# Kernel optimization log

Measured on AMD Instinct MI355X. Metric: run time of the kernel, lower is better.

## Reference

```python
import jax, jax.numpy as jnp
import numpy as np

N_NODES = 100000
N_EDGES = 1600000
N_GRAPHS = 64
NEG_SLOPE = 0.2


def gat_conv(x, W, att_src, att_dst, bias, edge_index, n_nodes, heads, out_ch, concat):
    """PyG-style GATConv (eval mode, self loops already included in edge_index)."""
    h = (x @ W).reshape(n_nodes, heads, out_ch)            # [N, H, C]
    a_src = jnp.einsum('nhc,hc->nh', h, att_src)           # [N, H]
    a_dst = jnp.einsum('nhc,hc->nh', h, att_dst)           # [N, H]
    src, dst = edge_index[0], edge_index[1]
    e = jax.nn.leaky_relu(a_src[src] + a_dst[dst], NEG_SLOPE)   # [E, H]
    # segment softmax over incoming edges of each destination node
    m = jax.ops.segment_max(e, dst, num_segments=n_nodes)      # [N, H]
    ex = jnp.exp(e - m[dst])
    denom = jax.ops.segment_sum(ex, dst, num_segments=n_nodes) # [N, H]
    alpha = ex / denom[dst]                                     # [E, H]
    msg = h[src] * alpha[:, :, None]                            # [E, H, C]
    out = jax.ops.segment_sum(msg, dst, num_segments=n_nodes)   # [N, H, C]
    if concat:
        out = out.reshape(n_nodes, heads * out_ch)
    else:
        out = out.mean(axis=1)
    return out + bias


def setup_inputs() -> dict:
    key = jax.random.key(0)
    ks = jax.random.split(key, 16)
    x = jax.random.normal(ks[0], (N_NODES, 1), dtype=jnp.float32)
    edge_index = jax.random.randint(ks[1], (2, N_EDGES), 0, N_NODES, dtype=jnp.int64)
    batch = jnp.sort(jax.random.randint(ks[2], (N_NODES,), 0, N_GRAPHS, dtype=jnp.int64))
    def glorot(k, shape):
        fan = (shape[0] + shape[-1])
        return jax.random.uniform(k, shape, jnp.float32, -1.0, 1.0) * np.sqrt(6.0 / fan)
    # layer 1: in=1, heads=8, out=8, concat
    W1 = glorot(ks[3], (1, 64))
    att_src1 = glorot(ks[4], (8, 8))
    att_dst1 = glorot(ks[5], (8, 8))
    b1 = jnp.zeros((64,), jnp.float32)
    # layer 2: in=64, heads=8, out=16, mean
    W2 = glorot(ks[6], (64, 128))
    att_src2 = glorot(ks[7], (8, 16))
    att_dst2 = glorot(ks[8], (8, 16))
    b2 = jnp.zeros((16,), jnp.float32)
    # fc 16 -> 4
    Wfc = glorot(ks[9], (16, 4))
    bfc = jnp.zeros((4,), jnp.float32)
    return dict(x=x, W1=W1, att_src1=att_src1, att_dst1=att_dst1, b1=b1,
                W2=W2, att_src2=att_src2, att_dst2=att_dst2, b2=b2,
                Wfc=Wfc, bfc=bfc, edge_index=edge_index, batch=batch)


def reference(x, W1, att_src1, att_dst1, b1, W2, att_src2, att_dst2, b2, Wfc, bfc, edge_index, batch):
    n = x.shape[0]
    # PyG GATConv default add_self_loops=True
    loops = jnp.arange(n, dtype=edge_index.dtype)
    ei = jnp.concatenate([edge_index, jnp.stack([loops, loops])], axis=1)
    h = gat_conv(x, W1, att_src1, att_dst1, b1, ei, n, heads=8, out_ch=8, concat=True)
    h = jax.nn.elu(h)
    # F.dropout(training=False) and attention dropout are no-ops in eval mode
    h = gat_conv(h, W2, att_src2, att_dst2, b2, ei, n, heads=8, out_ch=16, concat=False)
    # global mean pool over graphs
    sums = jax.ops.segment_sum(h, batch, num_segments=N_GRAPHS)          # [G, 16]
    cnts = jax.ops.segment_sum(jnp.ones((n,), h.dtype), batch, num_segments=N_GRAPHS)
    pooled = sums / jnp.maximum(cnts, 1.0)[:, None]
    return pooled @ Wfc + bfc                                            # [G, 4]
```

## Files before the change

kernel.cpp:

```cpp
#include <hip/hip_runtime.h>
#include <hip/hip_fp16.h>

#define N_NODES  100000
#define N_EDGES  1600000
#define N_GRAPHS 64

#define BINSH  8
#define NBIN   392
#define BINCAP 8192
#define EPB    2048
#define BUCKSH 13

__device__ __forceinline__ float lrelu(float v) { return v > 0.f ? v : 0.2f * v; }
__device__ __forceinline__ float elu_f(float v) { return v > 0.f ? v : __expf(v) - 1.f; }
__device__ __forceinline__ float rdlane_f(float v, int lane) {
    return __int_as_float(__builtin_amdgcn_readlane(__float_as_int(v), lane));
}

__global__ __launch_bounds__(512) void k_binA(
    const int* __restrict__ src, const int* __restrict__ dst,
    const int* __restrict__ batch, int* __restrict__ gbin_cursor,
    int* __restrict__ cnt, int2* __restrict__ binned) {
    __shared__ int hist[NBIN], lexcl[NBIN], runbase[NBIN], lcur[NBIN];
    __shared__ int wpart[8];
    __shared__ int gh[N_GRAPHS];
    __shared__ int2 stage[EPB];
    int t = threadIdx.x;
    int e0 = blockIdx.x * EPB;
    for (int b = t; b < NBIN; b += 512) hist[b] = 0;
    if (t < N_GRAPHS) gh[t] = 0;
    __syncthreads();
    int nid = blockIdx.x * 512 + t;
    if (nid < N_NODES) atomicAdd(&gh[batch[nid]], 1);
    int e = 4 * t;
    int4 dv = make_int4(0, 0, 0, 0), sv = make_int4(0, 0, 0, 0);
    bool full = (e0 + e + 3 < N_EDGES);
    if (full) {
        dv = *(const int4*)(dst + e0 + e);
        sv = *(const int4*)(src + e0 + e);
        atomicAdd(&hist[dv.x >> BINSH], 1);
        atomicAdd(&hist[dv.y >> BINSH], 1);
        atomicAdd(&hist[dv.z >> BINSH], 1);
        atomicAdd(&hist[dv.w >> BINSH], 1);
    } else {
        for (int k = 0; k < 4; ++k)
            if (e0 + e + k < N_EDGES) atomicAdd(&hist[dst[e0 + e + k] >> BINSH], 1);
    }
    __syncthreads();
    int v = (t < NBIN) ? hist[t] : 0;
    int x = v;
#pragma unroll
    for (int d = 1; d < 64; d <<= 1) {
        int y = __shfl_up(x, d, 64);
        if ((t & 63) >= d) x += y;
    }
    if ((t & 63) == 63) wpart[t >> 6] = x;
    __syncthreads();
    if (t == 0) {
        int a = 0;
        for (int w = 0; w < 8; ++w) { int q = wpart[w]; wpart[w] = a; a += q; }
    }
    __syncthreads();
    int excl = x - v + wpart[t >> 6];
    if (t < NBIN) { lexcl[t] = excl; lcur[t] = excl; }
    __syncthreads();
    if (t < NBIN && v > 0) runbase[t] = atomicAdd(&gbin_cursor[t], v);
    if (t < N_GRAPHS && gh[t]) atomicAdd(&cnt[t], gh[t]);
    __syncthreads();
    if (full) {
        int p;
        p = atomicAdd(&lcur[dv.x >> BINSH], 1); stage[p] = make_int2(sv.x, dv.x);
        p = atomicAdd(&lcur[dv.y >> BINSH], 1); stage[p] = make_int2(sv.y, dv.y);
        p = atomicAdd(&lcur[dv.z >> BINSH], 1); stage[p] = make_int2(sv.z, dv.z);
        p = atomicAdd(&lcur[dv.w >> BINSH], 1); stage[p] = make_int2(sv.w, dv.w);
    } else {
        for (int k = 0; k < 4; ++k) {
            if (e0 + e + k < N_EDGES) {
                int d = dst[e0 + e + k];
                int p = atomicAdd(&lcur[d >> BINSH], 1);
                stage[p] = make_int2(src[e0 + e + k], d);
            }
        }
    }
    __syncthreads();
    int m = N_EDGES - e0;
    if (m > EPB) m = EPB;
    for (int i = 4 * t; i < 4 * t + 4 && i < m; ++i) {
        int2 pr = stage[i];
        int b = pr.y >> BINSH;
        binned[(size_t)b * BINCAP + runbase[b] + (i - lexcl[b])] = pr;
    }
}

__global__ __launch_bounds__(1024) void k_binB(
    const int2* __restrict__ binned, const int* __restrict__ gbin_cursor,
    int* __restrict__ off, int* __restrict__ csr) {
    __shared__ int hist[4096];
    __shared__ int wpart[16];
    __shared__ int s_ebase;
    int b = blockIdx.x, t = threadIdx.x;
    int count = gbin_cursor[b];
    int node0 = b << BINSH;
    const int2* my = binned + (size_t)b * BINCAP;
    if (t == 0) s_ebase = 0;
    for (int i = t; i < 4096; i += 1024) hist[i] = 0;
    __syncthreads();
    if (t < b) atomicAdd(&s_ebase, gbin_cursor[t]);
    for (int i = t; i < count; i += 1024) {
        int2 pr = my[i];
        int key = ((pr.y - node0) << 4) | (pr.x >> BUCKSH);
        atomicAdd(&hist[key], 1);
    }
    __syncthreads();
    int v0 = hist[4 * t], v1 = hist[4 * t + 1], v2 = hist[4 * t + 2], v3 = hist[4 * t + 3];
    int s = v0 + v1 + v2 + v3;
    int x = s;
#pragma unroll
    for (int d = 1; d < 64; d <<= 1) {
        int y = __shfl_up(x, d, 64);
        if ((t & 63) >= d) x += y;
    }
    if ((t & 63) == 63) wpart[t >> 6] = x;
    __syncthreads();
    if (t == 0) {
        int a = 0;
        for (int w = 0; w < 16; ++w) { int q = wpart[w]; wpart[w] = a; a += q; }
    }
    __syncthreads();
    int base = x - s + wpart[t >> 6];
    hist[4 * t]     = base;
    hist[4 * t + 1] = base + v0;
    hist[4 * t + 2] = base + v0 + v1;
    hist[4 * t + 3] = base + v0 + v1 + v2;
    __syncthreads();
    int ebase = s_ebase;
    if (t < 256) {
        int n = node0 + t;
        if (n < N_NODES) off[n] = ebase + hist[t << 4];
    }
    if (b == 0 && t == 0) off[N_NODES] = N_EDGES;
    __syncthreads();
    for (int i = t; i < count; i += 1024) {
        int2 pr = my[i];
        int key = ((pr.y - node0) << 4) | (pr.x >> BUCKSH);
        int p = atomicAdd(&hist[key], 1);
        csr[ebase + p] = pr.x;
    }
}

__global__ __launch_bounds__(256) void k_l1gemm(
    const float* __restrict__ x, const float* __restrict__ W1,
    const float* __restrict__ as1, const float* __restrict__ ad1,
    const float* __restrict__ b1, const float* __restrict__ W2,
    const float* __restrict__ as2, const float* __restrict__ ad2,
    const int* __restrict__ off, const int* __restrict__ csr,
    __half2* __restrict__ h2p, float2* __restrict__ ap, float2* __restrict__ dp) {
    __shared__ float4 smW4[32 * 64];
    __shared__ float smS1[32][8];
    __shared__ float smws[8], smwd[8];
    int t = threadIdx.x;
    for (int idx = t; idx < 2048; idx += 256) {
        int k2 = idx >> 6, ll = idx & 63;
        smW4[idx] = make_float4(W2[(2 * k2) * 128 + ll], W2[(2 * k2) * 128 + 64 + ll],
                                W2[(2 * k2 + 1) * 128 + ll], W2[(2 * k2 + 1) * 128 + 64 + ll]);
    }
    if (t < 8) {
        float s = 0.f, d = 0.f;
        for (int c = 0; c < 8; ++c) {
            float w = W1[t * 8 + c];
            s += w * as1[t * 8 + c];
            d += w * ad1[t * 8 + c];
        }
        smws[t] = s;
        smwd[t] = d;
    }
    __syncthreads();

    {
        int c = t & 15;
        float ws[8], wd[8];
#pragma unroll
        for (int h = 0; h < 8; ++h) { ws[h] = smws[h]; wd[h] = smwd[h]; }
        for (int p = 0; p < 2; ++p) {
            int nl = p * 16 + (t >> 4);
            int n = blockIdx.x * 32 + nl;
            float xn = x[n];
            float num[8], den[8];
#pragma unroll
            for (int h = 0; h < 8; ++h) { num[h] = 0.f; den[h] = 0.f; }
            if (c == 0) {
#pragma unroll
                for (int h = 0; h < 8; ++h) {
                    float w = __expf(lrelu(xn * ws[h] + xn * wd[h]));
                    den[h] = w;
                    num[h] = w * xn;
                }
            }
            int bo = off[n], e = off[n + 1];
            for (int i = bo + c; i < e; i += 16) {
                int s = csr[i];
                float xs = x[s];
#pragma unroll
                for (int h = 0; h < 8; ++h) {
                    float w = __expf(lrelu(xs * ws[h] + xn * wd[h]));
                    den[h] += w;
                    num[h] += w * xs;
                }
            }
#pragma unroll
            for (int d = 1; d < 16; d <<= 1) {
#pragma unroll
                for (int h = 0; h < 8; ++h) {
                    num[h] += __shfl_xor(num[h], d, 64);
                    den[h] += __shfl_xor(den[h], d, 64);
                }
            }
            if (c == 0) {
#pragma unroll
                for (int h = 0; h < 8; ++h) smS1[nl][h] = num[h] / den[h];
            }
        }
    }
    __syncthreads();

    int wid = t >> 6, l = t & 63;
    float w1l = W1[l], b1l = b1[l];
    float asA = as2[l], asB = as2[64 + l], adA = ad2[l], adB = ad2[64 + l];
    for (int q = 0; q < 8; ++q) {
        int nl = wid * 8 + q;
        int n = blockIdx.x * 32 + nl;
        float a = elu_f(smS1[nl][l >> 3] * w1l + b1l);
        float acc0 = 0.f, acc1 = 0.f;
#pragma unroll
        for (int k2 = 0; k2 < 32; ++k2) {
            float4 wv = smW4[k2 * 64 + l];
            float a0 = rdlane_f(a, 2 * k2);
            float a1 = rdlane_f(a, 2 * k2 + 1);
            acc0 += a0 * wv.x + a1 * wv.z;
            acc1 += a0 * wv.y + a1 * wv.w;
        }
        h2p[n * 64 + l] = __floats2half2_rn(acc0, acc1);

        float pSA = acc0 * asA;
        float pSB = acc1 * asB;
        float pDA = acc0 * adA;
        float pDB = acc1 * adB;
#pragma unroll
        for (int d = 1; d < 16; d <<= 1) {
            pSA += __shfl_xor(pSA, d, 64);
            pSB += __shfl_xor(pSB, d, 64);
            pDA += __shfl_xor(pDA, d, 64);
            pDB += __shfl_xor(pDB, d, 64);
        }
        if ((l & 15) == 0) {
            int h = l >> 4;
            ap[n * 4 + h] = make_float2(pSA, pSB);
            dp[n * 4 + h] = make_float2(pDA, pDB);
        }
    }
}

__global__ __launch_bounds__(256, 8) void k_layer2(
    const __half2* __restrict__ h2p, const float2* __restrict__ ap,
    const float2* __restrict__ dp, const int* __restrict__ off,
    const int* __restrict__ csr, const int* __restrict__ batch,
    float* __restrict__ pool) {
    __shared__ float smv[4][16];
    __shared__ int smg[4];
    const float* apf = (const float*)ap;
    const float* dpf = (const float*)dp;
    int t = threadIdx.x;
    int wid = t >> 6, l = t & 63;
    int n = blockIdx.x * 4 + wid;
    int hA = l >> 4;
    int hh = l & 7;
    int j8 = l >> 3;
    int fidx = 2 * (hh & 3) + (hh >> 2);
    float dn = dpf[n * 8 + fidx];

    float2 ad = dp[n * 4 + hA];
    float2 an = ap[n * 4 + hA];
    float wA = __expf(lrelu(an.x + ad.x));
    float wB = __expf(lrelu(an.y + ad.y));
    float2 hn = __half22float2(h2p[n * 64 + l]);
    float accA = wA * hn.x, accB = wB * hn.y;
    float denTA = wA, denTB = wB;
    float wsum = 0.f;

    int b = off[n];
    int deg = off[n + 1] - b;
    for (int base = 0; base < deg; base += 64) {
        int rem = deg - base;
        if (rem > 64) rem = 64;
        int sl = (l < rem) ? csr[b + base + l] : 0;
        int g = 0;
        for (; g + 8 <= rem; g += 8) {
            int sg = __shfl(sl, g + j8, 64);
            float w = __expf(lrelu(apf[sg * 8 + fidx] + dn));
            wsum += w;
#pragma unroll
            for (int j2 = 0; j2 < 8; ++j2) {
                int s = __builtin_amdgcn_readlane(sl, g + j2);
                float wa = __shfl(w, j2 * 8 + hA, 64);
                float wb = __shfl(w, j2 * 8 + hA + 4, 64);
                float2 gg = __half22float2(h2p[s * 64 + l]);
                accA = fmaf(wa, gg.x, accA);
                accB = fmaf(wb, gg.y, accB);
            }
        }
        if (g < rem) {
            int cnt = rem - g;
            int jj = (j8 < cnt) ? j8 : 0;
            int sg = __shfl(sl, g + jj, 64);
            float w = (j8 < cnt) ? __expf(lrelu(apf[sg * 8 + fidx] + dn)) : 0.f;
            wsum += w;
            for (int j2 = 0; j2 < cnt; ++j2) {
                int s = __builtin_amdgcn_readlane(sl, g + j2);
                float wa = __shfl(w, j2 * 8 + hA, 64);
                float wb = __shfl(w, j2 * 8 + hA + 4, 64);
                float2 gg = __half22float2(h2p[s * 64 + l]);
                accA = fmaf(wa, gg.x, accA);
                accB = fmaf(wb, gg.y, accB);
            }
        }
    }
    wsum += __shfl_xor(wsum, 8, 64);
    wsum += __shfl_xor(wsum, 16, 64);
    wsum += __shfl_xor(wsum, 32, 64);
    float denA = denTA + __shfl(wsum, hA, 64);
    float denB = denTB + __shfl(wsum, hA + 4, 64);

    float v = accA / denA + accB / denB;
    v += __shfl_xor(v, 16, 64);
    v += __shfl_xor(v, 32, 64);
    v *= 0.125f;
    if (l < 16) smv[wid][l] = v;
    if (l == 0) smg[wid] = batch[n];
    __syncthreads();
    if (t < 64) {
        int w = t >> 4, c = t & 15;
        int g = smg[w];
        bool leader = true;
        for (int w2 = 0; w2 < w; ++w2)
            if (smg[w2] == g) { leader = false; break; }
        if (leader) {
            float s = smv[w][c];
            for (int w2 = w + 1; w2 < 4; ++w2)
                if (smg[w2] == g) s += smv[w2][c];
            atomicAdd(&pool[g * 16 + c], s);
        }
    }
}

__global__ void k_final(const float* __restrict__ pool, const int* __restrict__ cnt,
                        const float* __restrict__ b2, const float* __restrict__ Wfc,
                        const float* __restrict__ bfc, float* __restrict__ out) {
    int t = threadIdx.x;
    int g = t >> 2, k = t & 3;
    float c = (float)(cnt[g] > 0 ? cnt[g] : 1);
    float acc = bfc[k];
#pragma unroll
    for (int ci = 0; ci < 16; ++ci)
        acc += (pool[g * 16 + ci] / c + b2[ci]) * Wfc[ci * 4 + k];
    out[g * 4 + k] = acc;
}

extern "C" void kernel_launch(void* const* d_in, const int* in_sizes, int n_in,
                              void* d_out, int out_size, void* d_ws, size_t ws_size,
                              hipStream_t stream) {
    const float* x   = (const float*)d_in[0];
    const float* W1  = (const float*)d_in[1];
    const float* as1 = (const float*)d_in[2];
    const float* ad1 = (const float*)d_in[3];
    const float* b1  = (const float*)d_in[4];
    const float* W2  = (const float*)d_in[5];
    const float* as2 = (const float*)d_in[6];
    const float* ad2 = (const float*)d_in[7];
    const float* b2  = (const float*)d_in[8];
    const float* Wfc = (const float*)d_in[9];
    const float* bfc = (const float*)d_in[10];
    const int* ei    = (const int*)d_in[11];
    const int* batch = (const int*)d_in[12];
    const int* srcv  = ei;
    const int* dstv  = ei + N_EDGES;

    char* ws = (char*)d_ws;
    size_t o = 0;
    auto alloc = [&](size_t bytes) {
        void* p = ws + o;
        o += (bytes + 255) & ~(size_t)255;
        return p;
    };
    int*    cnt     = (int*)alloc(64 * 4);
    float*  pool    = (float*)alloc(64 * 16 * 4);
    int*    gbin    = (int*)alloc(NBIN * 4);
    size_t  zbytes  = o;
    int*    off     = (int*)alloc((size_t)(N_NODES + 1) * 4);
    int*    csr     = (int*)alloc((size_t)N_EDGES * 4);
    char*   ubase   = (char*)alloc((size_t)N_NODES * 64 * 4 + (size_t)N_NODES * 4 * 8 * 2);
    int2*   binned  = (int2*)ubase;
    __half2* h2p    = (__half2*)ubase;
    float2* ap      = (float2*)(ubase + (size_t)N_NODES * 64 * 4);
    float2* dp      = (float2*)(ubase + (size_t)N_NODES * 64 * 4 + (size_t)N_NODES * 4 * 8);

    hipMemsetAsync(d_ws, 0, zbytes, stream);

    int nbA = (N_EDGES + EPB - 1) / EPB;

    k_binA<<<nbA, 512, 0, stream>>>(srcv, dstv, batch, gbin, cnt, binned);
    k_binB<<<NBIN, 1024, 0, stream>>>(binned, gbin, off, csr);
    k_l1gemm<<<N_NODES / 32, 256, 0, stream>>>(x, W1, as1, ad1, b1, W2, as2, ad2,
                                               off, csr, h2p, ap, dp);
    k_layer2<<<N_NODES / 4, 256, 0, stream>>>(h2p, ap, dp, off, csr, batch, pool);
    k_final<<<1, 256, 0, stream>>>(pool, cnt, b2, Wfc, bfc, (float*)d_out);
}
```

Measured before the change: 307.1 us.

## Drop source-bucket sub-sort in CSR build and reuse W2 loads across eight nodes

The CSR bin kernel no longer sub-sorts edges by source bucket within each destination node. It now uses a 256-entry per-node histogram and a shorter scan, which cuts shared-memory size and scan work but loses the source locality that helped later gathers. The layer-1 GEMM is restructured so each W2 shared-memory load is reused across the eight nodes a wave processes, rather than being reloaded for each node. This reduces LDS traffic at the cost of more registers.

```diff
diff --git a/kernel.cpp b/kernel.cpp
--- a/kernel.cpp
+++ b/kernel.cpp
@@ -9,7 +9,6 @@
 #define NBIN   392
 #define BINCAP 8192
 #define EPB    2048
-#define BUCKSH 13
 
 __device__ __forceinline__ float lrelu(float v) { return v > 0.f ? v : 0.2f * v; }
 __device__ __forceinline__ float elu_f(float v) { return v > 0.f ? v : __expf(v) - 1.f; }
@@ -95,55 +94,46 @@
 __global__ __launch_bounds__(1024) void k_binB(
     const int2* __restrict__ binned, const int* __restrict__ gbin_cursor,
     int* __restrict__ off, int* __restrict__ csr) {
-    __shared__ int hist[4096];
-    __shared__ int wpart[16];
+    __shared__ int hist[256];
+    __shared__ int wpart[4];
     __shared__ int s_ebase;
     int b = blockIdx.x, t = threadIdx.x;
     int count = gbin_cursor[b];
     int node0 = b << BINSH;
     const int2* my = binned + (size_t)b * BINCAP;
     if (t == 0) s_ebase = 0;
-    for (int i = t; i < 4096; i += 1024) hist[i] = 0;
+    if (t < 256) hist[t] = 0;
     __syncthreads();
     if (t < b) atomicAdd(&s_ebase, gbin_cursor[t]);
-    for (int i = t; i < count; i += 1024) {
-        int2 pr = my[i];
-        int key = ((pr.y - node0) << 4) | (pr.x >> BUCKSH);
-        atomicAdd(&hist[key], 1);
-    }
-    __syncthreads();
-    int v0 = hist[4 * t], v1 = hist[4 * t + 1], v2 = hist[4 * t + 2], v3 = hist[4 * t + 3];
-    int s = v0 + v1 + v2 + v3;
-    int x = s;
+    for (int i = t; i < count; i += 1024) atomicAdd(&hist[my[i].y - node0], 1);
+    __syncthreads();
+    int v = (t < 256) ? hist[t] : 0;
+    int x = v;
 #pragma unroll
     for (int d = 1; d < 64; d <<= 1) {
         int y = __shfl_up(x, d, 64);
         if ((t & 63) >= d) x += y;
     }
-    if ((t & 63) == 63) wpart[t >> 6] = x;
+    if (t < 256 && (t & 63) == 63) wpart[t >> 6] = x;
     __syncthreads();
     if (t == 0) {
         int a = 0;
-        for (int w = 0; w < 16; ++w) { int q = wpart[w]; wpart[w] = a; a += q; }
-    }
-    __syncthreads();
-    int base = x - s + wpart[t >> 6];
-    hist[4 * t]     = base;
-    hist[4 * t + 1] = base + v0;
-    hist[4 * t + 2] = base + v0 + v1;
-    hist[4 * t + 3] = base + v0 + v1 + v2;
+        for (int w = 0; w < 4; ++w) { int q = wpart[w]; wpart[w] = a; a += q; }
+    }
     __syncthreads();
     int ebase = s_ebase;
+    int excl = x - v + ((t < 256) ? wpart[t >> 6] : 0);
     if (t < 256) {
         int n = node0 + t;
-        if (n < N_NODES) off[n] = ebase + hist[t << 4];
+        if (n < N_NODES) off[n] = ebase + excl;
     }
     if (b == 0 && t == 0) off[N_NODES] = N_EDGES;
+    __syncthreads();
+    if (t < 256) hist[t] = excl;
     __syncthreads();
     for (int i = t; i < count; i += 1024) {
         int2 pr = my[i];
-        int key = ((pr.y - node0) << 4) | (pr.x >> BUCKSH);
-        int p = atomicAdd(&hist[key], 1);
+        int p = atomicAdd(&hist[pr.y - node0], 1);
         csr[ebase + p] = pr.x;
     }
 }
@@ -225,26 +215,34 @@
 
     int wid = t >> 6, l = t & 63;
     float w1l = W1[l], b1l = b1[l];
+    float av[8], acc0[8], acc1[8];
+#pragma unroll
+    for (int q = 0; q < 8; ++q) {
+        av[q] = elu_f(smS1[wid * 8 + q][l >> 3] * w1l + b1l);
+        acc0[q] = 0.f;
+        acc1[q] = 0.f;
+    }
+#pragma unroll
+    for (int k2 = 0; k2 < 32; ++k2) {
+        float4 wv = smW4[k2 * 64 + l];
+#pragma unroll
+        for (int q = 0; q < 8; ++q) {
+            float a0 = rdlane_f(av[q], 2 * k2);
+            float a1 = rdlane_f(av[q], 2 * k2 + 1);
+            acc0[q] += a0 * wv.x + a1 * wv.z;
+            acc1[q] += a0 * wv.y + a1 * wv.w;
+        }
+    }
     float asA = as2[l], asB = as2[64 + l], adA = ad2[l], adB = ad2[64 + l];
+#pragma unroll
     for (int q = 0; q < 8; ++q) {
-        int nl = wid * 8 + q;
-        int n = blockIdx.x * 32 + nl;
-        float a = elu_f(smS1[nl][l >> 3] * w1l + b1l);
-        float acc0 = 0.f, acc1 = 0.f;
-#pragma unroll
-        for (int k2 = 0; k2 < 32; ++k2) {
-            float4 wv = smW4[k2 * 64 + l];
-            float a0 = rdlane_f(a, 2 * k2);
-            float a1 = rdlane_f(a, 2 * k2 + 1);
-            acc0 += a0 * wv.x + a1 * wv.z;
-            acc1 += a0 * wv.y + a1 * wv.w;
-        }
-        h2p[n * 64 + l] = __floats2half2_rn(acc0, acc1);
-
-        float pSA = acc0 * asA;
-        float pSB = acc1 * asB;
-        float pDA = acc0 * adA;
-        float pDB = acc1 * adB;
+        int n = blockIdx.x * 32 + wid * 8 + q;
+        h2p[n * 64 + l] = __floats2half2_rn(acc0[q], acc1[q]);
+
+        float pSA = acc0[q] * asA;
+        float pSB = acc1[q] * asB;
+        float pDA = acc0[q] * adA;
+        float pDB = acc1[q] * adB;
 #pragma unroll
         for (int d = 1; d < 16; d <<= 1) {
             pSA += __shfl_xor(pSA, d, 64);
```

New measurement: 355.2 us. 15.7% more time.
